# Kernel tuning notes

Measured on AMD Instinct MI355X. Metric: run time of the kernel, lower is better.

The kernel has to match this reference:

```python
import jax, jax.numpy as jnp
import numpy as np

N_NODES = 100000
N_EDGES = 1600000
IN_DIM = 128
OUT_DIM = 10
N_GRAPHS = 512


def setup_inputs() -> dict:
    key = jax.random.key(0)
    ks = jax.random.split(key, 16)
    x = jax.random.normal(ks[0], (N_NODES, IN_DIM), dtype=jnp.float32)
    edge_index = jax.random.randint(ks[1], (2, N_EDGES), 0, N_NODES, dtype=jnp.int64)
    batch = jnp.sort(jax.random.randint(ks[2], (N_NODES,), 0, N_GRAPHS, dtype=jnp.int64))
    s = 0.1
    params = {
        'W1': jax.random.normal(ks[3], (IN_DIM, 32), dtype=jnp.float32) * s,
        'b1': jnp.zeros((32,), dtype=jnp.float32),
        'W2': jax.random.normal(ks[4], (32, 64), dtype=jnp.float32) * s,
        'b2': jnp.zeros((64,), dtype=jnp.float32),
        'W3': jax.random.normal(ks[5], (64, 128), dtype=jnp.float32) * s,
        'b3': jnp.zeros((128,), dtype=jnp.float32),
        'Wl1': jax.random.normal(ks[6], (128, 64), dtype=jnp.float32) * s,
        'bl1': jnp.zeros((64,), dtype=jnp.float32),
        'Wl2': jax.random.normal(ks[7], (64, OUT_DIM), dtype=jnp.float32) * s,
        'bl2': jnp.zeros((OUT_DIM,), dtype=jnp.float32),
    }
    return {'x': x, 'edge_index': edge_index, 'batch': batch, **params}


def _gcn_conv(x, src, dst, norm, W, b, n):
    # PyG GCNConv: out[i] = sum_j norm_ij * (x[j] @ W) + b, with self-loops folded into (src, dst).
    xw = x @ W                                   # [N, F_out]
    msg = xw[src] * norm[:, None]                # gather + scale  [E+N, F_out]
    return jax.ops.segment_sum(msg, dst, num_segments=n) + b


def reference(x, edge_index, batch, W1, b1, W2, b2, W3, b3, Wl1, bl1, Wl2, bl2):
    n = x.shape[0]
    loops = jnp.arange(n, dtype=edge_index.dtype)
    src = jnp.concatenate([edge_index[0], loops])  # j (source)
    dst = jnp.concatenate([edge_index[1], loops])  # i (target)
    # symmetric normalization D^{-1/2} (A+I) D^{-1/2}; degree at targets incl. self-loops
    deg = jax.ops.segment_sum(jnp.ones_like(dst, dtype=x.dtype), dst, num_segments=n)
    dinv = jnp.where(deg > 0, jax.lax.rsqrt(deg), 0.0)
    norm = dinv[src] * dinv[dst]
    # eval mode: dropout is identity
    h = jax.nn.relu(_gcn_conv(x, src, dst, norm, W1, b1, n))
    h = jax.nn.relu(_gcn_conv(h, src, dst, norm, W2, b2, n))
    h = _gcn_conv(h, src, dst, norm, W3, b3, n)
    g = jax.ops.segment_sum(h, batch, num_segments=N_GRAPHS)  # global_add_pool
    g = jax.nn.relu(g @ Wl1 + bl1)
    g = g @ Wl2 + bl2
    return jax.nn.log_softmax(g, axis=1)
```

## Files before the change

kernel.cpp:

```cpp
#include <hip/hip_runtime.h>
#include <hip/hip_bf16.h>
#include <math.h>
#include <type_traits>

#define NN 100000
#define NE 1600000
#define NG 512
#define NPB 128
#define NBUCK ((NN + NPB - 1) / NPB)
#define BCAP 3072
#define PBLOCKS 256
#define PTHREADS 1024

__device__ __forceinline__ float b2f(ushort u){ return __uint_as_float(((unsigned int)u)<<16); }
__device__ __forceinline__ ushort f2b(float f){
    __hip_bfloat16 h = __float2bfloat16(f);
    return *(ushort*)&h;
}
__device__ __forceinline__ float blo(unsigned int u){ return __uint_as_float(u<<16); }
__device__ __forceinline__ float bhi(unsigned int u){ return __uint_as_float(u & 0xffff0000u); }
__device__ __forceinline__ void acc4(float* a, uint2 u){
    a[0] += blo(u.x); a[1] += bhi(u.x); a[2] += blo(u.y); a[3] += bhi(u.y);
}
__device__ __forceinline__ void acc8(float* a, uint4 u){
    a[0] += blo(u.x); a[1] += bhi(u.x); a[2] += blo(u.y); a[3] += bhi(u.y);
    a[4] += blo(u.z); a[5] += bhi(u.z); a[6] += blo(u.w); a[7] += bhi(u.w);
}

__global__ __launch_bounds__(PTHREADS) void part_kernel(const int* __restrict__ src, const int* __restrict__ dst,
                                                        int* __restrict__ bucket_cnt, int* __restrict__ recs, int e){
    __shared__ int hist[NBUCK];
    __shared__ int base_[NBUCK];
    int tid = threadIdx.x;
    for(int b=tid; b<NBUCK; b+=PTHREADS) hist[b]=0;
    __syncthreads();
    int per = (e + PBLOCKS - 1) / PBLOCKS;
    per = (per + 3) & ~3;
    int lo = blockIdx.x * per;
    int hi = lo + per; if(hi > e) hi = e;
    if(lo >= hi) return;
    const int4* __restrict__ dst4 = (const int4*)dst;
    const int4* __restrict__ src4 = (const int4*)src;
    for(int i=lo/4+tid; i<hi/4; i+=PTHREADS){
        int4 d = dst4[i];
        atomicAdd(&hist[d.x>>7], 1);
        atomicAdd(&hist[d.y>>7], 1);
        atomicAdd(&hist[d.z>>7], 1);
        atomicAdd(&hist[d.w>>7], 1);
    }
    __syncthreads();
    for(int b=tid; b<NBUCK; b+=PTHREADS){
        int h = hist[b];
        base_[b] = h ? atomicAdd(&bucket_cnt[b], h) : 0;
        hist[b] = 0;
    }
    __syncthreads();
    for(int i=lo/4+tid; i<hi/4; i+=PTHREADS){
        int4 d = dst4[i];
        int4 s = src4[i];
        int b0=d.x>>7, b1=d.y>>7, b2=d.z>>7, b3=d.w>>7;
        int p0 = base_[b0] + atomicAdd(&hist[b0],1);
        int p1 = base_[b1] + atomicAdd(&hist[b1],1);
        int p2 = base_[b2] + atomicAdd(&hist[b2],1);
        int p3 = base_[b3] + atomicAdd(&hist[b3],1);
        if(p0 < BCAP) recs[(size_t)b0*BCAP + p0] = ((d.x & 127) << 17) | s.x;
        if(p1 < BCAP) recs[(size_t)b1*BCAP + p1] = ((d.y & 127) << 17) | s.y;
        if(p2 < BCAP) recs[(size_t)b2*BCAP + p2] = ((d.z & 127) << 17) | s.z;
        if(p3 < BCAP) recs[(size_t)b3*BCAP + p3] = ((d.w & 127) << 17) | s.w;
    }
}

__global__ __launch_bounds__(1024) void bucket_csr_kernel(const int* __restrict__ recs, const int* __restrict__ bucket_cnt,
                                                          int* __restrict__ csr, int* __restrict__ row_start,
                                                          int* __restrict__ row_end, float* __restrict__ dinv, int n){
    __shared__ int sr[BCAP];
    __shared__ int h2[NPB*8];
    __shared__ int pc[NPB];
    __shared__ int hh[NPB];
    int b = blockIdx.x, tid = threadIdx.x;
    int cnt = bucket_cnt[b]; if(cnt > BCAP) cnt = BCAP;
    for(int i=tid; i<cnt; i+=1024) sr[i] = recs[(size_t)b*BCAP + i];
    h2[tid] = 0;
    __syncthreads();
    for(int i=tid; i<cnt; i+=1024){
        int rec = sr[i];
        atomicAdd(&h2[((rec>>17)<<3) | ((rec & 131071)>>14)], 1);
    }
    __syncthreads();
    if(tid < NPB){
        int s = 0;
        #pragma unroll
        for(int k=0;k<8;k++) s += h2[tid*8+k];
        hh[tid] = s;
        pc[tid] = (s+3)&~3;
    }
    __syncthreads();
    for(int off=1; off<NPB; off<<=1){
        int t = (tid>=off && tid<NPB) ? pc[tid-off] : 0;
        __syncthreads();
        if(tid<NPB) pc[tid] += t;
        __syncthreads();
    }
    if(tid < NPB){
        int hp = (hh[tid]+3)&~3;
        int excl = pc[tid] - hp;
        int run = excl;
        #pragma unroll
        for(int k=0;k<8;k++){ int c = h2[tid*8+k]; h2[tid*8+k] = run; run += c; }
        int node = b*NPB + tid;
        if(node < n){
            row_start[node] = b*BCAP + excl;
            row_end[node]   = b*BCAP + excl + hh[tid];
            dinv[node] = rsqrtf((float)(hh[tid] + 1));
        }
    }
    __syncthreads();
    for(int i=tid; i<cnt; i+=1024){
        int rec = sr[i];
        int src = rec & 131071;
        int p = atomicAdd(&h2[((rec>>17)<<3) | (src>>14)], 1);
        csr[(size_t)b*BCAP + p] = src;
    }
}

template<int K, int NCOL, int RPT, bool BIAS, bool RELU, bool SCALE, bool BF16IN, bool BF16OUT>
__global__ __launch_bounds__(256) void gemm_kernel(const void* __restrict__ X_, const float* __restrict__ W,
                                                   const float* __restrict__ bias, const float* __restrict__ dinv,
                                                   void* __restrict__ Y_, int n){
    using TX = typename std::conditional<BF16IN, ushort, float>::type;
    const TX* __restrict__ X = (const TX*)X_;
    constexpr int CG = NCOL/4;
    constexpr int RT = 256/CG;
    constexpr int ROWS = RT*RPT;
    __shared__ float sW[K*NCOL];
    for(int i=threadIdx.x; i<K*NCOL/4; i+=256)
        ((float4*)sW)[i] = ((const float4*)W)[i];
    __syncthreads();
    int cg = threadIdx.x % CG;
    int rt = threadIdx.x / CG;
    int base = blockIdx.x*ROWS + rt*RPT;
    float acc[RPT][4];
    #pragma unroll
    for(int j=0;j<RPT;j++){ acc[j][0]=0.f; acc[j][1]=0.f; acc[j][2]=0.f; acc[j][3]=0.f; }
    const TX* xp[RPT];
    #pragma unroll
    for(int j=0;j<RPT;j++){
        int r = base+j; if(r>n-1) r=n-1;
        xp[j] = X + (size_t)r*K;
    }
    for(int k4=0;k4<K/4;k4++){
        float4 w0 = *(const float4*)&sW[(k4*4+0)*NCOL + cg*4];
        float4 w1 = *(const float4*)&sW[(k4*4+1)*NCOL + cg*4];
        float4 w2 = *(const float4*)&sW[(k4*4+2)*NCOL + cg*4];
        float4 w3 = *(const float4*)&sW[(k4*4+3)*NCOL + cg*4];
        #pragma unroll
        for(int j=0;j<RPT;j++){
            float4 xv;
            if constexpr(BF16IN){
                ushort4 xu = ((const ushort4*)xp[j])[k4];
                xv = make_float4(b2f(xu.x), b2f(xu.y), b2f(xu.z), b2f(xu.w));
            } else {
                xv = ((const float4*)xp[j])[k4];
            }
            acc[j][0] += xv.x*w0.x + xv.y*w1.x + xv.z*w2.x + xv.w*w3.x;
            acc[j][1] += xv.x*w0.y + xv.y*w1.y + xv.z*w2.y + xv.w*w3.y;
            acc[j][2] += xv.x*w0.z + xv.y*w1.z + xv.z*w2.z + xv.w*w3.z;
            acc[j][3] += xv.x*w0.w + xv.y*w1.w + xv.z*w2.w + xv.w*w3.w;
        }
    }
    float4 bv = make_float4(0.f,0.f,0.f,0.f);
    if constexpr(BIAS) bv = *(const float4*)&bias[cg*4];
    #pragma unroll
    for(int j=0;j<RPT;j++){
        int r = base+j;
        if(r<n){
            float4 o;
            o.x = acc[j][0]+bv.x; o.y = acc[j][1]+bv.y;
            o.z = acc[j][2]+bv.z; o.w = acc[j][3]+bv.w;
            if constexpr(RELU){
                o.x=fmaxf(o.x,0.f); o.y=fmaxf(o.y,0.f);
                o.z=fmaxf(o.z,0.f); o.w=fmaxf(o.w,0.f);
            }
            if constexpr(SCALE){
                float s = dinv[r];
                o.x*=s; o.y*=s; o.z*=s; o.w*=s;
            }
            if constexpr(BF16OUT){
                ushort4 u = make_ushort4(f2b(o.x), f2b(o.y), f2b(o.z), f2b(o.w));
                *(ushort4*)&((ushort*)Y_)[(size_t)r*NCOL + cg*4] = u;
            } else {
                *(float4*)&((float*)Y_)[(size_t)r*NCOL + cg*4] = o;
            }
        }
    }
}

template<int F, bool BIAS, bool RELU, bool POSTSCALE>
__global__ __launch_bounds__(256) void prop_kernel(const ushort* __restrict__ xin, ushort* __restrict__ xout,
                                                   const int* __restrict__ csr, const int* __restrict__ row_start,
                                                   const int* __restrict__ row_end, const float* __restrict__ dinv,
                                                   const float* __restrict__ bias, int n){
    constexpr int L = F/8;
    int gt  = blockIdx.x*256 + threadIdx.x;
    int node = gt / L;
    int f4   = gt & (L-1);
    if(node>=n) return;
    float di = dinv[node];
    const uint4* __restrict__ xw = ((const uint4*)xin) + f4;
    float a[8] = {0.f,0.f,0.f,0.f,0.f,0.f,0.f,0.f};
    float b[8] = {0.f,0.f,0.f,0.f,0.f,0.f,0.f,0.f};
    acc8(a, xw[(size_t)node*L]);
    int e  = row_start[node];
    int ee = row_end[node];
    for(; e+7<ee; e+=8){
        int4 c0 = *(const int4*)&csr[e];
        int4 c1 = *(const int4*)&csr[e+4];
        uint4 u0 = xw[(size_t)c0.x*L];
        uint4 u1 = xw[(size_t)c0.y*L];
        uint4 u2 = xw[(size_t)c0.z*L];
        uint4 u3 = xw[(size_t)c0.w*L];
        uint4 u4 = xw[(size_t)c1.x*L];
        uint4 u5 = xw[(size_t)c1.y*L];
        uint4 u6 = xw[(size_t)c1.z*L];
        uint4 u7 = xw[(size_t)c1.w*L];
        acc8(a,u0); acc8(b,u1); acc8(a,u2); acc8(b,u3);
        acc8(a,u4); acc8(b,u5); acc8(a,u6); acc8(b,u7);
    }
    if(e+3<ee){
        int4 c0 = *(const int4*)&csr[e];
        uint4 u0 = xw[(size_t)c0.x*L];
        uint4 u1 = xw[(size_t)c0.y*L];
        uint4 u2 = xw[(size_t)c0.z*L];
        uint4 u3 = xw[(size_t)c0.w*L];
        acc8(a,u0); acc8(b,u1); acc8(a,u2); acc8(b,u3);
        e += 4;
    }
    for(; e<ee; ++e) acc8(a, xw[(size_t)csr[e]*L]);
    float r[8];
    #pragma unroll
    for(int j=0;j<8;j++){
        r[j] = di*(a[j]+b[j]);
        if constexpr(BIAS) r[j] += bias[8*f4+j];
        if constexpr(RELU) r[j] = fmaxf(r[j],0.f);
        if constexpr(POSTSCALE) r[j] *= di;
    }
    uint4 outu;
    outu.x = ((unsigned int)f2b(r[1])<<16) | (unsigned int)f2b(r[0]);
    outu.y = ((unsigned int)f2b(r[3])<<16) | (unsigned int)f2b(r[2]);
    outu.z = ((unsigned int)f2b(r[5])<<16) | (unsigned int)f2b(r[4]);
    outu.w = ((unsigned int)f2b(r[7])<<16) | (unsigned int)f2b(r[6]);
    ((uint4*)xout)[(size_t)node*L + f4] = outu;
}

__global__ __launch_bounds__(256) void prop_gemm_kernel(const ushort* __restrict__ xin, ushort* __restrict__ xout,
                                                        const int* __restrict__ csr, const int* __restrict__ row_start,
                                                        const int* __restrict__ row_end, const float* __restrict__ dinv,
                                                        const float* __restrict__ W2, const float* __restrict__ b2, int n){
    __shared__ float4 sW2v[32*16];
    for(int i=threadIdx.x; i<512; i+=256) sW2v[i] = ((const float4*)W2)[i];
    __syncthreads();
    int gt  = blockIdx.x*256 + threadIdx.x;
    int node = gt >> 3;
    int og   = gt & 7;
    if(node >= n) return;
    float di = dinv[node];
    const uint2* __restrict__ xw = ((const uint2*)xin) + og;
    float a[4] = {0.f,0.f,0.f,0.f};
    float b[4] = {0.f,0.f,0.f,0.f};
    acc4(a, xw[(size_t)node*8]);
    int e  = row_start[node];
    int ee = row_end[node];
    for(; e+7<ee; e+=8){
        int4 c0 = *(const int4*)&csr[e];
        int4 c1 = *(const int4*)&csr[e+4];
        uint2 u0 = xw[(size_t)c0.x*8];
        uint2 u1 = xw[(size_t)c0.y*8];
        uint2 u2 = xw[(size_t)c0.z*8];
        uint2 u3 = xw[(size_t)c0.w*8];
        uint2 u4 = xw[(size_t)c1.x*8];
        uint2 u5 = xw[(size_t)c1.y*8];
        uint2 u6 = xw[(size_t)c1.z*8];
        uint2 u7 = xw[(size_t)c1.w*8];
        acc4(a,u0); acc4(b,u1); acc4(a,u2); acc4(b,u3);
        acc4(a,u4); acc4(b,u5); acc4(a,u6); acc4(b,u7);
    }
    if(e+3<ee){
        int4 c0 = *(const int4*)&csr[e];
        uint2 u0 = xw[(size_t)c0.x*8];
        uint2 u1 = xw[(size_t)c0.y*8];
        uint2 u2 = xw[(size_t)c0.z*8];
        uint2 u3 = xw[(size_t)c0.w*8];
        acc4(a,u0); acc4(b,u1); acc4(a,u2); acc4(b,u3);
        e += 4;
    }
    for(; e<ee; ++e) acc4(a, xw[(size_t)csr[e]*8]);
    float r[4];
    r[0] = di*(a[0]+b[0]);
    r[1] = di*(a[1]+b[1]);
    r[2] = di*(a[2]+b[2]);
    r[3] = di*(a[3]+b[3]);
    float acc[8] = {0.f,0.f,0.f,0.f,0.f,0.f,0.f,0.f};
    #pragma unroll
    for(int k=0;k<32;k++){
        float s = __shfl(r[k&3], k>>2, 8);
        float4 wa = sW2v[k*16 + og*2];
        float4 wb = sW2v[k*16 + og*2 + 1];
        acc[0]+=s*wa.x; acc[1]+=s*wa.y; acc[2]+=s*wa.z; acc[3]+=s*wa.w;
        acc[4]+=s*wb.x; acc[5]+=s*wb.y; acc[6]+=s*wb.z; acc[7]+=s*wb.w;
    }
    float4 ba = *(const float4*)&b2[og*8];
    float4 bb = *(const float4*)&b2[og*8+4];
    float o0 = di*fmaxf(acc[0]+ba.x, 0.f);
    float o1 = di*fmaxf(acc[1]+ba.y, 0.f);
    float o2 = di*fmaxf(acc[2]+ba.z, 0.f);
    float o3 = di*fmaxf(acc[3]+ba.w, 0.f);
    float o4 = di*fmaxf(acc[4]+bb.x, 0.f);
    float o5 = di*fmaxf(acc[5]+bb.y, 0.f);
    float o6 = di*fmaxf(acc[6]+bb.z, 0.f);
    float o7 = di*fmaxf(acc[7]+bb.w, 0.f);
    uint4 u;
    u.x = ((unsigned int)f2b(o1)<<16) | (unsigned int)f2b(o0);
    u.y = ((unsigned int)f2b(o3)<<16) | (unsigned int)f2b(o2);
    u.z = ((unsigned int)f2b(o5)<<16) | (unsigned int)f2b(o4);
    u.w = ((unsigned int)f2b(o7)<<16) | (unsigned int)f2b(o6);
    ((uint4*)xout)[(size_t)node*8 + og] = u;
}

__global__ __launch_bounds__(256) void prop_pool_kernel(const ushort* __restrict__ xin,
                                                        const int* __restrict__ csr, const int* __restrict__ row_start,
                                                        const int* __restrict__ row_end, const float* __restrict__ dinv,
                                                        const int* __restrict__ batch, float* __restrict__ pool, int n){
    __shared__ float sp[32*64];
    __shared__ int sg[32];
    int base = blockIdx.x*32;
    int tid = threadIdx.x;
    int node = base + (tid >> 3);
    int f4 = tid & 7;
    if(tid < 32) sg[tid] = batch[base+tid];
    float di = dinv[node];
    const uint4* __restrict__ xw = ((const uint4*)xin) + f4;
    float a[8] = {0.f,0.f,0.f,0.f,0.f,0.f,0.f,0.f};
    float b[8] = {0.f,0.f,0.f,0.f,0.f,0.f,0.f,0.f};
    acc8(a, xw[(size_t)node*8]);
    int e  = row_start[node];
    int ee = row_end[node];
    for(; e+7<ee; e+=8){
        int4 c0 = *(const int4*)&csr[e];
        int4 c1 = *(const int4*)&csr[e+4];
        uint4 u0 = xw[(size_t)c0.x*8];
        uint4 u1 = xw[(size_t)c0.y*8];
        uint4 u2 = xw[(size_t)c0.z*8];
        uint4 u3 = xw[(size_t)c0.w*8];
        uint4 u4 = xw[(size_t)c1.x*8];
        uint4 u5 = xw[(size_t)c1.y*8];
        uint4 u6 = xw[(size_t)c1.z*8];
        uint4 u7 = xw[(size_t)c1.w*8];
        acc8(a,u0); acc8(b,u1); acc8(a,u2); acc8(b,u3);
        acc8(a,u4); acc8(b,u5); acc8(a,u6); acc8(b,u7);
    }
    if(e+3<ee){
        int4 c0 = *(const int4*)&csr[e];
        uint4 u0 = xw[(size_t)c0.x*8];
        uint4 u1 = xw[(size_t)c0.y*8];
        uint4 u2 = xw[(size_t)c0.z*8];
        uint4 u3 = xw[(size_t)c0.w*8];
        acc8(a,u0); acc8(b,u1); acc8(a,u2); acc8(b,u3);
        e += 4;
    }
    for(; e<ee; ++e) acc8(a, xw[(size_t)csr[e]*8]);
    float4 r0, r1;
    r0.x = di*(a[0]+b[0]); r0.y = di*(a[1]+b[1]); r0.z = di*(a[2]+b[2]); r0.w = di*(a[3]+b[3]);
    r1.x = di*(a[4]+b[4]); r1.y = di*(a[5]+b[5]); r1.z = di*(a[6]+b[6]); r1.w = di*(a[7]+b[7]);
    ((float4*)sp)[tid*2]   = r0;
    ((float4*)sp)[tid*2+1] = r1;
    __syncthreads();
    if(tid < 64){
        int g0 = sg[0], g1 = sg[31];
        for(int g=g0; g<=g1; ++g){
            float s = 0.f;
            #pragma unroll
            for(int nl=0; nl<32; ++nl)
                if(sg[nl]==g) s += sp[nl*64 + tid];
            atomicAdd(&pool[g*64 + tid], s);
        }
    }
}

__global__ __launch_bounds__(128) void head_kernel(const float* __restrict__ pool, const int* __restrict__ batch, int n,
                                                   const float* __restrict__ W3, const float* __restrict__ b3,
                                                   const float* __restrict__ Wl1, const float* __restrict__ bl1,
                                                   const float* __restrict__ Wl2, const float* __restrict__ bl2,
                                                   float* __restrict__ out){
    __shared__ float sp[64];
    __shared__ float sg3[128];
    __shared__ float sh[64];
    __shared__ float sl[10];
    int g = blockIdx.x, t = threadIdx.x;
    if(t<64) sp[t] = pool[g*64+t];
    __syncthreads();
    int lo=0, hi=n;
    while(lo<hi){ int mid=(lo+hi)>>1; if(batch[mid]<g) lo=mid+1; else hi=mid; }
    int start=lo;
    lo=start; hi=n;
    while(lo<hi){ int mid=(lo+hi)>>1; if(batch[mid]<g+1) lo=mid+1; else hi=mid; }
    float cf = (float)(lo - start);
    float a = cf*b3[t];
    #pragma unroll 8
    for(int k=0;k<64;k++) a += sp[k]*W3[k*128+t];
    sg3[t]=a; __syncthreads();
    if(t<64){
        float h = bl1[t];
        #pragma unroll 8
        for(int k=0;k<128;k++) h += sg3[k]*Wl1[k*64+t];
        sh[t] = fmaxf(h,0.f);
    }
    __syncthreads();
    if(t<10){
        float l = bl2[t];
        for(int k=0;k<64;k++) l += sh[k]*Wl2[k*10+t];
        sl[t]=l;
    }
    __syncthreads();
    if(t<10){
        float m=sl[0];
        for(int k=1;k<10;k++) m=fmaxf(m,sl[k]);
        float s=0.f;
        for(int k=0;k<10;k++) s+=expf(sl[k]-m);
        out[g*10+t] = sl[t]-m-logf(s);
    }
}

extern "C" void kernel_launch(void* const* d_in, const int* in_sizes, int n_in,
                              void* d_out, int out_size, void* d_ws, size_t ws_size,
                              hipStream_t stream){
    const float* x   = (const float*)d_in[0];
    const int*   ei  = (const int*)d_in[1];
    const int* batch = (const int*)d_in[2];
    const float* W1  = (const float*)d_in[3];
    const float* b1  = (const float*)d_in[4];
    const float* W2  = (const float*)d_in[5];
    const float* b2  = (const float*)d_in[6];
    const float* W3  = (const float*)d_in[7];
    const float* b3  = (const float*)d_in[8];
    const float* Wl1 = (const float*)d_in[9];
    const float* bl1 = (const float*)d_in[10];
    const float* Wl2 = (const float*)d_in[11];
    const float* bl2 = (const float*)d_in[12];
    const int n = NN, E = NE;
    const int* src = ei;
    const int* dst = ei + E;

    char* ws = (char*)d_ws;
    size_t off = 0;
    auto alloc = [&](size_t bytes)->char*{
        char* p = ws + off;
        off = (off + bytes + 255) & ~(size_t)255;
        return p;
    };
    int*    bucket_cnt = (int*)   alloc((size_t)NBUCK*4);
    float*  pool       = (float*) alloc((size_t)NG*64*4);
    size_t  zero_bytes = (size_t)((char*)pool - (char*)bucket_cnt) + (size_t)NG*64*4;
    float*  dinv       = (float*) alloc((size_t)n*4);
    int*    recs       = (int*)   alloc((size_t)NBUCK*BCAP*4);
    int*    csr        = (int*)   alloc((size_t)NBUCK*BCAP*4);
    int*    row_start  = (int*)   alloc((size_t)n*4);
    int*    row_end    = (int*)   alloc((size_t)n*4);
    ushort* y1         = (ushort*)alloc((size_t)n*32*2);
    ushort* h1y        = (ushort*)alloc((size_t)n*32*2);
    ushort* h2y        = (ushort*)alloc((size_t)n*64*2);

    hipMemsetAsync(bucket_cnt, 0, zero_bytes, stream);
    part_kernel<<<PBLOCKS,PTHREADS,0,stream>>>(src, dst, bucket_cnt, recs, E);
    bucket_csr_kernel<<<NBUCK,1024,0,stream>>>(recs, bucket_cnt, csr, row_start, row_end, dinv, n);

    gemm_kernel<128,32,2,false,false,true,false,true><<<(n+63)/64,256,0,stream>>>(x, W1, nullptr, dinv, y1, n);
    prop_kernel<32,true,true,true><<<(n*4+255)/256,256,0,stream>>>(y1, h1y, csr, row_start, row_end, dinv, b1, n);
    prop_gemm_kernel<<<(n*8+255)/256,256,0,stream>>>(h1y, h2y, csr, row_start, row_end, dinv, W2, b2, n);
    prop_pool_kernel<<<(n+31)/32,256,0,stream>>>(h2y, csr, row_start, row_end, dinv, batch, pool, n);
    head_kernel<<<NG,128,0,stream>>>(pool, batch, n, W3, b3, Wl1, bl1, Wl2, bl2, (float*)d_out);
}
```

Before: 255.4 us.

## Fuse first GEMM into partition kernel and pad CSR rows with dummy node

Runs the unscaled layer-1 GEMM (x@W1) in extra blocks of the edge-partition kernel so the two independent stages overlap in one launch. The dinv scaling of y1 moves into the bucket CSR kernel. CSR rows are padded to a multiple of four with a dummy zero node NN, so the propagation loops drop their scalar tail and prefetch the next index quads. This cuts kernel launches and per-row branching, at the cost of extra rows, padding writes and a larger, mixed-role merged kernel.

```diff
diff --git a/kernel.cpp b/kernel.cpp
--- a/kernel.cpp
+++ b/kernel.cpp
@@ -1,7 +1,6 @@
 #include <hip/hip_runtime.h>
 #include <hip/hip_bf16.h>
 #include <math.h>
-#include <type_traits>
 
 #define NN 100000
 #define NE 1600000
@@ -10,7 +9,7 @@
 #define NBUCK ((NN + NPB - 1) / NPB)
 #define BCAP 3072
 #define PBLOCKS 256
-#define PTHREADS 1024
+#define GBLKS ((NN + 1 + 255) / 256)
 
 __device__ __forceinline__ float b2f(ushort u){ return __uint_as_float(((unsigned int)u)<<16); }
 __device__ __forceinline__ ushort f2b(float f){
@@ -27,56 +26,103 @@
     a[4] += blo(u.z); a[5] += bhi(u.z); a[6] += blo(u.w); a[7] += bhi(u.w);
 }
 
-__global__ __launch_bounds__(PTHREADS) void part_kernel(const int* __restrict__ src, const int* __restrict__ dst,
-                                                        int* __restrict__ bucket_cnt, int* __restrict__ recs, int e){
+__global__ __launch_bounds__(1024) void merged_kernel(const int* __restrict__ src, const int* __restrict__ dst,
+                                                      int* __restrict__ bucket_cnt, int* __restrict__ recs, int e,
+                                                      const float* __restrict__ x, const float* __restrict__ W1,
+                                                      ushort* __restrict__ y1){
     __shared__ int hist[NBUCK];
     __shared__ int base_[NBUCK];
+    __shared__ float sW[128*32];
     int tid = threadIdx.x;
-    for(int b=tid; b<NBUCK; b+=PTHREADS) hist[b]=0;
-    __syncthreads();
-    int per = (e + PBLOCKS - 1) / PBLOCKS;
-    per = (per + 3) & ~3;
-    int lo = blockIdx.x * per;
-    int hi = lo + per; if(hi > e) hi = e;
-    if(lo >= hi) return;
-    const int4* __restrict__ dst4 = (const int4*)dst;
-    const int4* __restrict__ src4 = (const int4*)src;
-    for(int i=lo/4+tid; i<hi/4; i+=PTHREADS){
-        int4 d = dst4[i];
-        atomicAdd(&hist[d.x>>7], 1);
-        atomicAdd(&hist[d.y>>7], 1);
-        atomicAdd(&hist[d.z>>7], 1);
-        atomicAdd(&hist[d.w>>7], 1);
-    }
-    __syncthreads();
-    for(int b=tid; b<NBUCK; b+=PTHREADS){
-        int h = hist[b];
-        base_[b] = h ? atomicAdd(&bucket_cnt[b], h) : 0;
-        hist[b] = 0;
-    }
-    __syncthreads();
-    for(int i=lo/4+tid; i<hi/4; i+=PTHREADS){
-        int4 d = dst4[i];
-        int4 s = src4[i];
-        int b0=d.x>>7, b1=d.y>>7, b2=d.z>>7, b3=d.w>>7;
-        int p0 = base_[b0] + atomicAdd(&hist[b0],1);
-        int p1 = base_[b1] + atomicAdd(&hist[b1],1);
-        int p2 = base_[b2] + atomicAdd(&hist[b2],1);
-        int p3 = base_[b3] + atomicAdd(&hist[b3],1);
-        if(p0 < BCAP) recs[(size_t)b0*BCAP + p0] = ((d.x & 127) << 17) | s.x;
-        if(p1 < BCAP) recs[(size_t)b1*BCAP + p1] = ((d.y & 127) << 17) | s.y;
-        if(p2 < BCAP) recs[(size_t)b2*BCAP + p2] = ((d.z & 127) << 17) | s.z;
-        if(p3 < BCAP) recs[(size_t)b3*BCAP + p3] = ((d.w & 127) << 17) | s.w;
+    if(blockIdx.x < PBLOCKS){
+        for(int b=tid; b<NBUCK; b+=1024) hist[b]=0;
+        __syncthreads();
+        int per = (e + PBLOCKS - 1) / PBLOCKS;
+        per = (per + 3) & ~3;
+        int lo = blockIdx.x * per;
+        int hi = lo + per; if(hi > e) hi = e;
+        if(lo >= hi) return;
+        const int4* __restrict__ dst4 = (const int4*)dst;
+        const int4* __restrict__ src4 = (const int4*)src;
+        for(int i=lo/4+tid; i<hi/4; i+=1024){
+            int4 d = dst4[i];
+            atomicAdd(&hist[d.x>>7], 1);
+            atomicAdd(&hist[d.y>>7], 1);
+            atomicAdd(&hist[d.z>>7], 1);
+            atomicAdd(&hist[d.w>>7], 1);
+        }
+        __syncthreads();
+        for(int b=tid; b<NBUCK; b+=1024){
+            int h = hist[b];
+            base_[b] = h ? atomicAdd(&bucket_cnt[b], h) : 0;
+            hist[b] = 0;
+        }
+        __syncthreads();
+        for(int i=lo/4+tid; i<hi/4; i+=1024){
+            int4 d = dst4[i];
+            int4 s = src4[i];
+            int b0=d.x>>7, b1=d.y>>7, b2=d.z>>7, b3=d.w>>7;
+            int p0 = base_[b0] + atomicAdd(&hist[b0],1);
+            int p1 = base_[b1] + atomicAdd(&hist[b1],1);
+            int p2 = base_[b2] + atomicAdd(&hist[b2],1);
+            int p3 = base_[b3] + atomicAdd(&hist[b3],1);
+            if(p0 < BCAP) recs[(size_t)b0*BCAP + p0] = ((d.x & 127) << 17) | s.x;
+            if(p1 < BCAP) recs[(size_t)b1*BCAP + p1] = ((d.y & 127) << 17) | s.y;
+            if(p2 < BCAP) recs[(size_t)b2*BCAP + p2] = ((d.z & 127) << 17) | s.z;
+            if(p3 < BCAP) recs[(size_t)b3*BCAP + p3] = ((d.w & 127) << 17) | s.w;
+        }
+    } else {
+        int gblk = blockIdx.x - PBLOCKS;
+        ((float4*)sW)[tid] = ((const float4*)W1)[tid];
+        __syncthreads();
+        int cg = tid & 7;
+        int rt = tid >> 3;
+        int base = gblk*256 + rt*2;
+        int r0 = base;   if(r0 > NN-1) r0 = NN-1;
+        int r1 = base+1; if(r1 > NN-1) r1 = NN-1;
+        const float* __restrict__ xp0 = x + (size_t)r0*128;
+        const float* __restrict__ xp1 = x + (size_t)r1*128;
+        float acc0[4] = {0.f,0.f,0.f,0.f};
+        float acc1[4] = {0.f,0.f,0.f,0.f};
+        for(int k4=0;k4<32;k4++){
+            float4 w0 = *(const float4*)&sW[(k4*4+0)*32 + cg*4];
+            float4 w1 = *(const float4*)&sW[(k4*4+1)*32 + cg*4];
+            float4 w2 = *(const float4*)&sW[(k4*4+2)*32 + cg*4];
+            float4 w3 = *(const float4*)&sW[(k4*4+3)*32 + cg*4];
+            float4 xa = ((const float4*)xp0)[k4];
+            float4 xb = ((const float4*)xp1)[k4];
+            acc0[0] += xa.x*w0.x + xa.y*w1.x + xa.z*w2.x + xa.w*w3.x;
+            acc0[1] += xa.x*w0.y + xa.y*w1.y + xa.z*w2.y + xa.w*w3.y;
+            acc0[2] += xa.x*w0.z + xa.y*w1.z + xa.z*w2.z + xa.w*w3.z;
+            acc0[3] += xa.x*w0.w + xa.y*w1.w + xa.z*w2.w + xa.w*w3.w;
+            acc1[0] += xb.x*w0.x + xb.y*w1.x + xb.z*w2.x + xb.w*w3.x;
+            acc1[1] += xb.x*w0.y + xb.y*w1.y + xb.z*w2.y + xb.w*w3.y;
+            acc1[2] += xb.x*w0.z + xb.y*w1.z + xb.z*w2.z + xb.w*w3.z;
+            acc1[3] += xb.x*w0.w + xb.y*w1.w + xb.z*w2.w + xb.w*w3.w;
+        }
+        #pragma unroll
+        for(int j=0;j<2;j++){
+            int r = base+j;
+            if(r <= NN){
+                float* a = j ? acc1 : acc0;
+                ushort4 u;
+                if(r == NN){ u = make_ushort4(0,0,0,0); }
+                else u = make_ushort4(f2b(a[0]), f2b(a[1]), f2b(a[2]), f2b(a[3]));
+                *(ushort4*)&y1[(size_t)r*32 + cg*4] = u;
+            }
+        }
     }
 }
 
 __global__ __launch_bounds__(1024) void bucket_csr_kernel(const int* __restrict__ recs, const int* __restrict__ bucket_cnt,
                                                           int* __restrict__ csr, int* __restrict__ row_start,
-                                                          int* __restrict__ row_end, float* __restrict__ dinv, int n){
+                                                          int* __restrict__ row_end, float* __restrict__ dinv,
+                                                          ushort* __restrict__ y1, int n){
     __shared__ int sr[BCAP];
     __shared__ int h2[NPB*8];
     __shared__ int pc[NPB];
     __shared__ int hh[NPB];
+    __shared__ float sdv[NPB];
     int b = blockIdx.x, tid = threadIdx.x;
     int cnt = bucket_cnt[b]; if(cnt > BCAP) cnt = BCAP;
     for(int i=tid; i<cnt; i+=1024) sr[i] = recs[(size_t)b*BCAP + i];
@@ -102,7 +148,8 @@
         __syncthreads();
     }
     if(tid < NPB){
-        int hp = (hh[tid]+3)&~3;
+        int h = hh[tid];
+        int hp = (h+3)&~3;
         int excl = pc[tid] - hp;
         int run = excl;
         #pragma unroll
@@ -110,190 +157,184 @@
         int node = b*NPB + tid;
         if(node < n){
             row_start[node] = b*BCAP + excl;
-            row_end[node]   = b*BCAP + excl + hh[tid];
-            dinv[node] = rsqrtf((float)(hh[tid] + 1));
+            row_end[node]   = b*BCAP + excl + hp;
+            float dv = rsqrtf((float)(h + 1));
+            dinv[node] = dv;
+            sdv[tid] = dv;
+            for(int k=h; k<hp; k++) csr[(size_t)b*BCAP + excl + k] = NN;
         }
     }
     __syncthreads();
     for(int i=tid; i<cnt; i+=1024){
         int rec = sr[i];
-        int src = rec & 131071;
-        int p = atomicAdd(&h2[((rec>>17)<<3) | (src>>14)], 1);
-        csr[(size_t)b*BCAP + p] = src;
-    }
-}
-
-template<int K, int NCOL, int RPT, bool BIAS, bool RELU, bool SCALE, bool BF16IN, bool BF16OUT>
-__global__ __launch_bounds__(256) void gemm_kernel(const void* __restrict__ X_, const float* __restrict__ W,
-                                                   const float* __restrict__ bias, const float* __restrict__ dinv,
-                                                   void* __restrict__ Y_, int n){
-    using TX = typename std::conditional<BF16IN, ushort, float>::type;
-    const TX* __restrict__ X = (const TX*)X_;
-    constexpr int CG = NCOL/4;
-    constexpr int RT = 256/CG;
-    constexpr int ROWS = RT*RPT;
-    __shared__ float sW[K*NCOL];
-    for(int i=threadIdx.x; i<K*NCOL/4; i+=256)
-        ((float4*)sW)[i] = ((const float4*)W)[i];
-    __syncthreads();
-    int cg = threadIdx.x % CG;
-    int rt = threadIdx.x / CG;
-    int base = blockIdx.x*ROWS + rt*RPT;
-    float acc[RPT][4];
-    #pragma unroll
-    for(int j=0;j<RPT;j++){ acc[j][0]=0.f; acc[j][1]=0.f; acc[j][2]=0.f; acc[j][3]=0.f; }
-    const TX* xp[RPT];
-    #pragma unroll
-    for(int j=0;j<RPT;j++){
-        int r = base+j; if(r>n-1) r=n-1;
-        xp[j] = X + (size_t)r*K;
-    }
-    for(int k4=0;k4<K/4;k4++){
-        float4 w0 = *(const float4*)&sW[(k4*4+0)*NCOL + cg*4];
-        float4 w1 = *(const float4*)&sW[(k4*4+1)*NCOL + cg*4];
-        float4 w2 = *(const float4*)&sW[(k4*4+2)*NCOL + cg*4];
-        float4 w3 = *(const float4*)&sW[(k4*4+3)*NCOL + cg*4];
-        #pragma unroll
-        for(int j=0;j<RPT;j++){
-            float4 xv;
-            if constexpr(BF16IN){
-                ushort4 xu = ((const ushort4*)xp[j])[k4];
-                xv = make_float4(b2f(xu.x), b2f(xu.y), b2f(xu.z), b2f(xu.w));
-            } else {
-                xv = ((const float4*)xp[j])[k4];
-            }
-            acc[j][0] += xv.x*w0.x + xv.y*w1.x + xv.z*w2.x + xv.w*w3.x;
-            acc[j][1] += xv.x*w0.y + xv.y*w1.y + xv.z*w2.y + xv.w*w3.y;
-            acc[j][2] += xv.x*w0.z + xv.y*w1.z + xv.z*w2.z + xv.w*w3.z;
-            acc[j][3] += xv.x*w0.w + xv.y*w1.w + xv.z*w2.w + xv.w*w3.w;
-        }
-    }
-    float4 bv = make_float4(0.f,0.f,0.f,0.f);
-    if constexpr(BIAS) bv = *(const float4*)&bias[cg*4];
-    #pragma unroll
-    for(int j=0;j<RPT;j++){
-        int r = base+j;
-        if(r<n){
-            float4 o;
-            o.x = acc[j][0]+bv.x; o.y = acc[j][1]+bv.y;
-            o.z = acc[j][2]+bv.z; o.w = acc[j][3]+bv.w;
-            if constexpr(RELU){
-                o.x=fmaxf(o.x,0.f); o.y=fmaxf(o.y,0.f);
-                o.z=fmaxf(o.z,0.f); o.w=fmaxf(o.w,0.f);
-            }
-            if constexpr(SCALE){
-                float s = dinv[r];
-                o.x*=s; o.y*=s; o.z*=s; o.w*=s;
-            }
-            if constexpr(BF16OUT){
-                ushort4 u = make_ushort4(f2b(o.x), f2b(o.y), f2b(o.z), f2b(o.w));
-                *(ushort4*)&((ushort*)Y_)[(size_t)r*NCOL + cg*4] = u;
-            } else {
-                *(float4*)&((float*)Y_)[(size_t)r*NCOL + cg*4] = o;
-            }
-        }
-    }
-}
-
-template<int F, bool BIAS, bool RELU, bool POSTSCALE>
-__global__ __launch_bounds__(256) void prop_kernel(const ushort* __restrict__ xin, ushort* __restrict__ xout,
-                                                   const int* __restrict__ csr, const int* __restrict__ row_start,
-                                                   const int* __restrict__ row_end, const float* __restrict__ dinv,
-                                                   const float* __restrict__ bias, int n){
-    constexpr int L = F/8;
+        int s = rec & 131071;
+        int p = atomicAdd(&h2[((rec>>17)<<3) | (s>>14)], 1);
+        csr[(size_t)b*BCAP + p] = s;
+    }
+    if(tid < 512){
+        int nl = tid >> 2;
+        int node = b*NPB + nl;
+        if(node < n){
+            float dv = sdv[nl];
+            uint4* yp = (uint4*)y1;
+            uint4 v = yp[(size_t)node*4 + (tid&3)];
+            float t0=blo(v.x)*dv, t1=bhi(v.x)*dv, t2=blo(v.y)*dv, t3=bhi(v.y)*dv;
+            float t4=blo(v.z)*dv, t5=bhi(v.z)*dv, t6=blo(v.w)*dv, t7=bhi(v.w)*dv;
+            uint4 o;
+            o.x = ((unsigned int)f2b(t1)<<16) | (unsigned int)f2b(t0);
+            o.y = ((unsigned int)f2b(t3)<<16) | (unsigned int)f2b(t2);
+            o.z = ((unsigned int)f2b(t5)<<16) | (unsigned int)f2b(t4);
+            o.w = ((unsigned int)f2b(t7)<<16) | (unsigned int)f2b(t6);
+            yp[(size_t)node*4 + (tid&3)] = o;
+        }
+    }
+}
+
+__global__ __launch_bounds__(256) void prop1_kernel(const ushort* __restrict__ xin, ushort* __restrict__ xout,
+                                                    const int* __restrict__ csr, const int* __restrict__ row_start,
+                                                    const int* __restrict__ row_end, const float* __restrict__ dinv,
+                                                    const float* __restrict__ bias){
     int gt  = blockIdx.x*256 + threadIdx.x;
-    int node = gt / L;
-    int f4   = gt & (L-1);
-    if(node>=n) return;
+    int node = gt >> 2;
+    int f4   = gt & 3;
+    if(node > NN) return;
+    if(node == NN){ ((uint4*)xout)[(size_t)NN*4 + f4] = make_uint4(0,0,0,0); return; }
     float di = dinv[node];
     const uint4* __restrict__ xw = ((const uint4*)xin) + f4;
     float a[8] = {0.f,0.f,0.f,0.f,0.f,0.f,0.f,0.f};
     float b[8] = {0.f,0.f,0.f,0.f,0.f,0.f,0.f,0.f};
-    acc8(a, xw[(size_t)node*L]);
+    acc8(a, xw[(size_t)node*4]);
     int e  = row_start[node];
-    int ee = row_end[node];
-    for(; e+7<ee; e+=8){
-        int4 c0 = *(const int4*)&csr[e];
-        int4 c1 = *(const int4*)&csr[e+4];
-        uint4 u0 = xw[(size_t)c0.x*L];
-        uint4 u1 = xw[(size_t)c0.y*L];
-        uint4 u2 = xw[(size_t)c0.z*L];
-        uint4 u3 = xw[(size_t)c0.w*L];
-        uint4 u4 = xw[(size_t)c1.x*L];
-        uint4 u5 = xw[(size_t)c1.y*L];
-        uint4 u6 = xw[(size_t)c1.z*L];
-        uint4 u7 = xw[(size_t)c1.w*L];
+    const int* __restrict__ cb = csr + e;
+    int nq = (row_end[node] - e) >> 2;
+    if(nq >= 2){
+        int4 c0 = *(const int4*)(cb);
+        int4 c1 = *(const int4*)(cb+4);
+        int q = 2;
+        for(; q+1 < nq; q += 2){
+            int4 n0 = *(const int4*)(cb+4*q);
+            int4 n1 = *(const int4*)(cb+4*q+4);
+            uint4 u0 = xw[(size_t)c0.x*4];
+            uint4 u1 = xw[(size_t)c0.y*4];
+            uint4 u2 = xw[(size_t)c0.z*4];
+            uint4 u3 = xw[(size_t)c0.w*4];
+            uint4 u4 = xw[(size_t)c1.x*4];
+            uint4 u5 = xw[(size_t)c1.y*4];
+            uint4 u6 = xw[(size_t)c1.z*4];
+            uint4 u7 = xw[(size_t)c1.w*4];
+            acc8(a,u0); acc8(b,u1); acc8(a,u2); acc8(b,u3);
+            acc8(a,u4); acc8(b,u5); acc8(a,u6); acc8(b,u7);
+            c0 = n0; c1 = n1;
+        }
+        {
+            uint4 u0 = xw[(size_t)c0.x*4];
+            uint4 u1 = xw[(size_t)c0.y*4];
+            uint4 u2 = xw[(size_t)c0.z*4];
+            uint4 u3 = xw[(size_t)c0.w*4];
+            uint4 u4 = xw[(size_t)c1.x*4];
+            uint4 u5 = xw[(size_t)c1.y*4];
+            uint4 u6 = xw[(size_t)c1.z*4];
+            uint4 u7 = xw[(size_t)c1.w*4];
+            acc8(a,u0); acc8(b,u1); acc8(a,u2); acc8(b,u3);
+            acc8(a,u4); acc8(b,u5); acc8(a,u6); acc8(b,u7);
+        }
+        if(q < nq){
+            int4 c = *(const int4*)(cb+4*q);
+            uint4 u0 = xw[(size_t)c.x*4];
+            uint4 u1 = xw[(size_t)c.y*4];
+            uint4 u2 = xw[(size_t)c.z*4];
+            uint4 u3 = xw[(size_t)c.w*4];
+            acc8(a,u0); acc8(b,u1); acc8(a,u2); acc8(b,u3);
+        }
+    } else if(nq == 1){
+        int4 c = *(const int4*)(cb);
+        uint4 u0 = xw[(size_t)c.x*4];
+        uint4 u1 = xw[(size_t)c.y*4];
+        uint4 u2 = xw[(size_t)c.z*4];
+        uint4 u3 = xw[(size_t)c.w*4];
         acc8(a,u0); acc8(b,u1); acc8(a,u2); acc8(b,u3);
-        acc8(a,u4); acc8(b,u5); acc8(a,u6); acc8(b,u7);
-    }
-    if(e+3<ee){
-        int4 c0 = *(const int4*)&csr[e];
-        uint4 u0 = xw[(size_t)c0.x*L];
-        uint4 u1 = xw[(size_t)c0.y*L];
-        uint4 u2 = xw[(size_t)c0.z*L];
-        uint4 u3 = xw[(size_t)c0.w*L];
-        acc8(a,u0); acc8(b,u1); acc8(a,u2); acc8(b,u3);
-        e += 4;
-    }
-    for(; e<ee; ++e) acc8(a, xw[(size_t)csr[e]*L]);
+    }
     float r[8];
     #pragma unroll
     for(int j=0;j<8;j++){
-        r[j] = di*(a[j]+b[j]);
-        if constexpr(BIAS) r[j] += bias[8*f4+j];
-        if constexpr(RELU) r[j] = fmaxf(r[j],0.f);
-        if constexpr(POSTSCALE) r[j] *= di;
+        r[j] = di*(a[j]+b[j]) + bias[8*f4+j];
+        r[j] = fmaxf(r[j],0.f) * di;
     }
     uint4 outu;
     outu.x = ((unsigned int)f2b(r[1])<<16) | (unsigned int)f2b(r[0]);
     outu.y = ((unsigned int)f2b(r[3])<<16) | (unsigned int)f2b(r[2]);
     outu.z = ((unsigned int)f2b(r[5])<<16) | (unsigned int)f2b(r[4]);
     outu.w = ((unsigned int)f2b(r[7])<<16) | (unsigned int)f2b(r[6]);
-    ((uint4*)xout)[(size_t)node*L + f4] = outu;
+    ((uint4*)xout)[(size_t)node*4 + f4] = outu;
 }
 
 __global__ __launch_bounds__(256) void prop_gemm_kernel(const ushort* __restrict__ xin, ushort* __restrict__ xout,
                                                         const int* __restrict__ csr, const int* __restrict__ row_start,
                                                         const int* __restrict__ row_end, const float* __restrict__ dinv,
-                                                        const float* __restrict__ W2, const float* __restrict__ b2, int n){
+                                                        const float* __restrict__ W2, const float* __restrict__ b2){
     __shared__ float4 sW2v[32*16];
     for(int i=threadIdx.x; i<512; i+=256) sW2v[i] = ((const float4*)W2)[i];
     __syncthreads();
     int gt  = blockIdx.x*256 + threadIdx.x;
     int node = gt >> 3;
     int og   = gt & 7;
-    if(node >= n) return;
+    if(node > NN) return;
+    if(node == NN){ ((uint4*)xout)[(size_t)NN*8 + og] = make_uint4(0,0,0,0); return; }
     float di = dinv[node];
     const uint2* __restrict__ xw = ((const uint2*)xin) + og;
     float a[4] = {0.f,0.f,0.f,0.f};
     float b[4] = {0.f,0.f,0.f,0.f};
     acc4(a, xw[(size_t)node*8]);
     int e  = row_start[node];
-    int ee = row_end[node];
-    for(; e+7<ee; e+=8){
-        int4 c0 = *(const int4*)&csr[e];
-        int4 c1 = *(const int4*)&csr[e+4];
-        uint2 u0 = xw[(size_t)c0.x*8];
-        uint2 u1 = xw[(size_t)c0.y*8];
-        uint2 u2 = xw[(size_t)c0.z*8];
-        uint2 u3 = xw[(size_t)c0.w*8];
-        uint2 u4 = xw[(size_t)c1.x*8];
-        uint2 u5 = xw[(size_t)c1.y*8];
-        uint2 u6 = xw[(size_t)c1.z*8];
-        uint2 u7 = xw[(size_t)c1.w*8];
+    const int* __restrict__ cb = csr + e;
+    int nq = (row_end[node] - e) >> 2;
+    if(nq >= 2){
+        int4 c0 = *(const int4*)(cb);
+        int4 c1 = *(const int4*)(cb+4);
+        int q = 2;
+        for(; q+1 < nq; q += 2){
+            int4 n0 = *(const int4*)(cb+4*q);
+            int4 n1 = *(const int4*)(cb+4*q+4);
+            uint2 u0 = xw[(size_t)c0.x*8];
+            uint2 u1 = xw[(size_t)c0.y*8];
+            uint2 u2 = xw[(size_t)c0.z*8];
+            uint2 u3 = xw[(size_t)c0.w*8];
+            uint2 u4 = xw[(size_t)c1.x*8];
+            uint2 u5 = xw[(size_t)c1.y*8];
+            uint2 u6 = xw[(size_t)c1.z*8];
+            uint2 u7 = xw[(size_t)c1.w*8];
+            acc4(a,u0); acc4(b,u1); acc4(a,u2); acc4(b,u3);
+            acc4(a,u4); acc4(b,u5); acc4(a,u6); acc4(b,u7);
+            c0 = n0; c1 = n1;
+        }
+        {
+            uint2 u0 = xw[(size_t)c0.x*8];
+            uint2 u1 = xw[(size_t)c0.y*8];
+            uint2 u2 = xw[(size_t)c0.z*8];
+            uint2 u3 = xw[(size_t)c0.w*8];
+            uint2 u4 = xw[(size_t)c1.x*8];
+            uint2 u5 = xw[(size_t)c1.y*8];
+            uint2 u6 = xw[(size_t)c1.z*8];
+            uint2 u7 = xw[(size_t)c1.w*8];
+            acc4(a,u0); acc4(b,u1); acc4(a,u2); acc4(b,u3);
+            acc4(a,u4); acc4(b,u5); acc4(a,u6); acc4(b,u7);
+        }
+        if(q < nq){
+            int4 c = *(const int4*)(cb+4*q);
+            uint2 u0 = xw[(size_t)c.x*8];
+            uint2 u1 = xw[(size_t)c.y*8];
+            uint2 u2 = xw[(size_t)c.z*8];
+            uint2 u3 = xw[(size_t)c.w*8];
+            acc4(a,u0); acc4(b,u1); acc4(a,u2); acc4(b,u3);
+        }
+    } else if(nq == 1){
+        int4 c = *(const int4*)(cb);
+        uint2 u0 = xw[(size_t)c.x*8];
+        uint2 u1 = xw[(size_t)c.y*8];
+        uint2 u2 = xw[(size_t)c.z*8];
+        uint2 u3 = xw[(size_t)c.w*8];
         acc4(a,u0); acc4(b,u1); acc4(a,u2); acc4(b,u3);
-        acc4(a,u4); acc4(b,u5); acc4(a,u6); acc4(b,u7);
-    }
-    if(e+3<ee){
-        int4 c0 = *(const int4*)&csr[e];
-        uint2 u0 = xw[(size_t)c0.x*8];
-        uint2 u1 = xw[(size_t)c0.y*8];
-        uint2 u2 = xw[(size_t)c0.z*8];
-        uint2 u3 = xw[(size_t)c0.w*8];
-        acc4(a,u0); acc4(b,u1); acc4(a,u2); acc4(b,u3);
-        e += 4;
-    }
-    for(; e<ee; ++e) acc4(a, xw[(size_t)csr[e]*8]);
+    }
     float r[4];
     r[0] = di*(a[0]+b[0]);
     r[1] = di*(a[1]+b[1]);
@@ -329,7 +370,7 @@
 __global__ __launch_bounds__(256) void prop_pool_kernel(const ushort* __restrict__ xin,
                                                         const int* __restrict__ csr, const int* __restrict__ row_start,
                                                         const int* __restrict__ row_end, const float* __restrict__ dinv,
-                                                        const int* __restrict__ batch, float* __restrict__ pool, int n){
+                                                        const int* __restrict__ batch, float* __restrict__ pool){
     __shared__ float sp[32*64];
     __shared__ int sg[32];
     int base = blockIdx.x*32;
@@ -343,31 +384,55 @@
     float b[8] = {0.f,0.f,0.f,0.f,0.f,0.f,0.f,0.f};
     acc8(a, xw[(size_t)node*8]);
     int e  = row_start[node];
-    int ee = row_end[node];
-    for(; e+7<ee; e+=8){
-        int4 c0 = *(const int4*)&csr[e];
-        int4 c1 = *(const int4*)&csr[e+4];
-        uint4 u0 = xw[(size_t)c0.x*8];
-        uint4 u1 = xw[(size_t)c0.y*8];
-        uint4 u2 = xw[(size_t)c0.z*8];
-        uint4 u3 = xw[(size_t)c0.w*8];
-        uint4 u4 = xw[(size_t)c1.x*8];
-        uint4 u5 = xw[(size_t)c1.y*8];
-        uint4 u6 = xw[(size_t)c1.z*8];
-        uint4 u7 = xw[(size_t)c1.w*8];
+    const int* __restrict__ cb = csr + e;
+    int nq = (row_end[node] - e) >> 2;
+    if(nq >= 2){
+        int4 c0 = *(const int4*)(cb);
+        int4 c1 = *(const int4*)(cb+4);
+        int q = 2;
+        for(; q+1 < nq; q += 2){
+            int4 n0 = *(const int4*)(cb+4*q);
+            int4 n1 = *(const int4*)(cb+4*q+4);
+            uint4 u0 = xw[(size_t)c0.x*8];
+            uint4 u1 = xw[(size_t)c0.y*8];
+            uint4 u2 = xw[(size_t)c0.z*8];
+            uint4 u3 = xw[(size_t)c0.w*8];
+            uint4 u4 = xw[(size_t)c1.x*8];
+            uint4 u5 = xw[(size_t)c1.y*8];
+            uint4 u6 = xw[(size_t)c1.z*8];
+            uint4 u7 = xw[(size_t)c1.w*8];
+            acc8(a,u0); acc8(b,u1); acc8(a,u2); acc8(b,u3);
+            acc8(a,u4); acc8(b,u5); acc8(a,u6); acc8(b,u7);
+            c0 = n0; c1 = n1;
+        }
+        {
+            uint4 u0 = xw[(size_t)c0.x*8];
+            uint4 u1 = xw[(size_t)c0.y*8];
+            uint4 u2 = xw[(size_t)c0.z*8];
+            uint4 u3 = xw[(size_t)c0.w*8];
+            uint4 u4 = xw[(size_t)c1.x*8];
+            uint4 u5 = xw[(size_t)c1.y*8];
+            uint4 u6 = xw[(size_t)c1.z*8];
+            uint4 u7 = xw[(size_t)c1.w*8];
+            acc8(a,u0); acc8(b,u1); acc8(a,u2); acc8(b,u3);
+            acc8(a,u4); acc8(b,u5); acc8(a,u6); acc8(b,u7);
+        }
+        if(q < nq){
+            int4 c = *(const int4*)(cb+4*q);
+            uint4 u0 = xw[(size_t)c.x*8];
+            uint4 u1 = xw[(size_t)c.y*8];
+            uint4 u2 = xw[(size_t)c.z*8];
+            uint4 u3 = xw[(size_t)c.w*8];
+            acc8(a,u0); acc8(b,u1); acc8(a,u2); acc8(b,u3);
+        }
+    } else if(nq == 1){
+        int4 c = *(const int4*)(cb);
+        uint4 u0 = xw[(size_t)c.x*8];
+        uint4 u1 = xw[(size_t)c.y*8];
+        uint4 u2 = xw[(size_t)c.z*8];
+        uint4 u3 = xw[(size_t)c.w*8];
         acc8(a,u0); acc8(b,u1); acc8(a,u2); acc8(b,u3);
-        acc8(a,u4); acc8(b,u5); acc8(a,u6); acc8(b,u7);
-    }
-    if(e+3<ee){
-        int4 c0 = *(const int4*)&csr[e];
-        uint4 u0 = xw[(size_t)c0.x*8];
-        uint4 u1 = xw[(size_t)c0.y*8];
-        uint4 u2 = xw[(size_t)c0.z*8];
-        uint4 u3 = xw[(size_t)c0.w*8];
-        acc8(a,u0); acc8(b,u1); acc8(a,u2); acc8(b,u3);
-        e += 4;
-    }
-    for(; e<ee; ++e) acc8(a, xw[(size_t)csr[e]*8]);
+    }
     float4 r0, r1;
     r0.x = di*(a[0]+b[0]); r0.y = di*(a[1]+b[1]); r0.z = di*(a[2]+b[2]); r0.w = di*(a[3]+b[3]);
     r1.x = di*(a[4]+b[4]); r1.y = di*(a[5]+b[5]); r1.z = di*(a[6]+b[6]); r1.w = di*(a[7]+b[7]);
@@ -465,17 +530,15 @@
     int*    csr        = (int*)   alloc((size_t)NBUCK*BCAP*4);
     int*    row_start  = (int*)   alloc((size_t)n*4);
     int*    row_end    = (int*)   alloc((size_t)n*4);
-    ushort* y1         = (ushort*)alloc((size_t)n*32*2);
-    ushort* h1y        = (ushort*)alloc((size_t)n*32*2);
-    ushort* h2y        = (ushort*)alloc((size_t)n*64*2);
+    ushort* y1         = (ushort*)alloc((size_t)(n+1)*32*2);
+    ushort* h1y        = (ushort*)alloc((size_t)(n+1)*32*2);
+    ushort* h2y        = (ushort*)alloc((size_t)(n+1)*64*2);
 
     hipMemsetAsync(bucket_cnt, 0, zero_bytes, stream);
-    part_kernel<<<PBLOCKS,PTHREADS,0,stream>>>(src, dst, bucket_cnt, recs, E);
-    bucket_csr_kernel<<<NBUCK,1024,0,stream>>>(recs, bucket_cnt, csr, row_start, row_end, dinv, n);
-
-    gemm_kernel<128,32,2,false,false,true,false,true><<<(n+63)/64,256,0,stream>>>(x, W1, nullptr, dinv, y1, n);
-    prop_kernel<32,true,true,true><<<(n*4+255)/256,256,0,stream>>>(y1, h1y, csr, row_start, row_end, dinv, b1, n);
-    prop_gemm_kernel<<<(n*8+255)/256,256,0,stream>>>(h1y, h2y, csr, row_start, row_end, dinv, W2, b2, n);
-    prop_pool_kernel<<<(n+31)/32,256,0,stream>>>(h2y, csr, row_start, row_end, dinv, batch, pool, n);
+    merged_kernel<<<PBLOCKS+GBLKS,1024,0,stream>>>(src, dst, bucket_cnt, recs, E, x, W1, y1);
+    bucket_csr_kernel<<<NBUCK,1024,0,stream>>>(recs, bucket_cnt, csr, row_start, row_end, dinv, y1, n);
+    prop1_kernel<<<((n+1)*4+255)/256,256,0,stream>>>(y1, h1y, csr, row_start, row_end, dinv, b1);
+    prop_gemm_kernel<<<((n+1)*8+255)/256,256,0,stream>>>(h1y, h2y, csr, row_start, row_end, dinv, W2, b2);
+    prop_pool_kernel<<<n/32,256,0,stream>>>(h2y, csr, row_start, row_end, dinv, batch, pool);
     head_kernel<<<NG,128,0,stream>>>(pool, batch, n, W3, b3, Wl1, bl1, Wl2, bl2, (float*)d_out);
 }
```

Result: faster. 249.7 us (median of 2 runs) (-2.2%).
